# Performance work log

Hardware: AMD Instinct MI355X
Metric: run time of the kernel (lower is better)

## Reference

```python
import jax, jax.numpy as jnp
import numpy as np

N, D_IN = 65536, 512
H1, H2, D_SH = 1024, 1024, 512   # shared net: num_nodes_shared = [1024, 1024, 512]
HI = 512                          # indiv hidden width, num_nodes_indiv = [512, 512]


def setup_inputs() -> dict:
    key = jax.random.key(0)
    ks = jax.random.split(key, 16)
    s = 0.02
    inp = {
        "input": jax.random.normal(ks[0], (N, D_IN), jnp.float32),
        "treatment": jax.random.randint(ks[1], (N,), 0, 2, jnp.int32),
        # shared net (hidden ReLU layers + linear output, all with bias)
        "W0": jax.random.normal(ks[2], (D_IN, H1), jnp.float32) * s,
        "b0": jnp.zeros((H1,), jnp.float32),
        "W1": jax.random.normal(ks[3], (H1, H2), jnp.float32) * s,
        "b1": jnp.zeros((H2,), jnp.float32),
        "W2": jax.random.normal(ks[4], (H2, D_SH), jnp.float32) * s,
        "b2": jnp.zeros((D_SH,), jnp.float32),
        # risk net 0 (output layer has no bias)
        "A0": jax.random.normal(ks[5], (D_SH, HI), jnp.float32) * s,
        "a0": jnp.zeros((HI,), jnp.float32),
        "A1": jax.random.normal(ks[6], (HI, HI), jnp.float32) * s,
        "a1": jnp.zeros((HI,), jnp.float32),
        "A2": jax.random.normal(ks[7], (HI, 1), jnp.float32) * s,
        # risk net 1
        "C0": jax.random.normal(ks[8], (D_SH, HI), jnp.float32) * s,
        "c0": jnp.zeros((HI,), jnp.float32),
        "C1": jax.random.normal(ks[9], (HI, HI), jnp.float32) * s,
        "c1": jnp.zeros((HI,), jnp.float32),
        "C2": jax.random.normal(ks[10], (HI, 1), jnp.float32) * s,
    }
    return inp


def _risk_net(h, U0, u0, U1, u1, U2):
    h = jax.nn.relu(h @ U0 + u0)
    h = jax.nn.relu(h @ U1 + u1)
    return h @ U2  # [N, 1], no output bias


def reference(input, treatment, W0, b0, W1, b1, W2, b2,
              A0, a0, A1, a1, A2, C0, c0, C1, c1, C2):
    # shared MLP
    h = jax.nn.relu(input @ W0 + b0)
    h = jax.nn.relu(h @ W1 + b1)
    out = h @ W2 + b2                     # [N, D_SH]
    # Binary expert routing. The torch code gathers samples per treatment,
    # runs each group through its own MLP and scatters results back; the
    # math is equivalent to applying both experts and selecting per sample.
    y0 = _risk_net(out, A0, a0, A1, a1, A2)[:, 0]  # [N]
    y1 = _risk_net(out, C0, c0, C1, c1, C2)[:, 0]  # [N]
    y = jnp.where(treatment == 0, y0, y1)          # [N]
    return (y, out)
```

## Files before the change

### kernel.cpp

```cpp
#include <hip/hip_runtime.h>
#include <hip/hip_bf16.h>
#include <stdint.h>

typedef short short8 __attribute__((ext_vector_type(8)));
typedef float f32x4 __attribute__((ext_vector_type(4)));

#define NSAMP 65536

__device__ __forceinline__ unsigned short f2bf(float f) {
    union { float f; unsigned u; } v; v.f = f;
    unsigned u = v.u;
    u += 0x7fffu + ((u >> 16) & 1u);
    return (unsigned short)(u >> 16);
}


__global__ void k_convert_bf16(const float* __restrict__ in, unsigned short* __restrict__ out, int n8) {
    int i = blockIdx.x * blockDim.x + threadIdx.x;
    if (i >= n8) return;
    const float4* p = (const float4*)in + (size_t)i * 2;
    float4 a = p[0], b = p[1];
    short8 o;
    o[0] = (short)f2bf(a.x); o[1] = (short)f2bf(a.y);
    o[2] = (short)f2bf(a.z); o[3] = (short)f2bf(a.w);
    o[4] = (short)f2bf(b.x); o[5] = (short)f2bf(b.y);
    o[6] = (short)f2bf(b.z); o[7] = (short)f2bf(b.w);
    ((short8*)out)[i] = o;
}

struct PrepArgs {
    const float *W0, *W1, *W2, *A0, *C0, *A1, *C1, *a0v, *c0v;
    unsigned short *W0T, *W1T, *W2T, *RT0, *A1T, *C1T;
    float *bcat, *y0, *y1;
};
__global__ void k_prep(PrepArgs p) {
    int i = blockIdx.x * blockDim.x + threadIdx.x;
    if (i < 524288)  { int k = i >> 10, n = i & 1023; p.W0T[n * 512 + k] = f2bf(p.W0[i]); return; }
    i -= 524288;
    if (i < 1048576) { int k = i >> 10, n = i & 1023; p.W1T[n * 1024 + k] = f2bf(p.W1[i]); return; }
    i -= 1048576;
    if (i < 524288)  { int k = i >> 9, n = i & 511; p.W2T[n * 1024 + k] = f2bf(p.W2[i]); return; }
    i -= 524288;
    if (i < 262144)  { int k = i >> 9, n = i & 511; p.RT0[n * 512 + k] = f2bf(p.A0[i]); return; }
    i -= 262144;
    if (i < 262144)  { int k = i >> 9, n = i & 511; p.RT0[(512 + n) * 512 + k] = f2bf(p.C0[i]); return; }
    i -= 262144;
    if (i < 262144)  { int k = i >> 9, n = i & 511; p.A1T[n * 512 + k] = f2bf(p.A1[i]); return; }
    i -= 262144;
    if (i < 262144)  { int k = i >> 9, n = i & 511; p.C1T[n * 512 + k] = f2bf(p.C1[i]); return; }
    i -= 262144;
    if (i < 512)     { p.bcat[i] = p.a0v[i]; return; }
    i -= 512;
    if (i < 512)     { p.bcat[512 + i] = p.c0v[i]; return; }
    i -= 512;
    if (i < 65536)   { p.y0[i] = 0.f; return; }
    i -= 65536;
    if (i < 65536)   { p.y1[i] = 0.f; return; }
}

__global__ void k_select(const float* __restrict__ y0, const float* __restrict__ y1,
                         const int* __restrict__ t, float* __restrict__ y, int n) {
    int i = blockIdx.x * blockDim.x + threadIdx.x;
    if (i < n) y[i] = (t[i] == 0) ? y0[i] : y1[i];
}

template<int MODE>
__global__ __launch_bounds__(512, 2)
void k_gemm256(const unsigned short* __restrict__ A, int lda, int colOff,
               const unsigned short* __restrict__ BT,
               const float* __restrict__ bias,
               unsigned short* __restrict__ Cbf,
               float* __restrict__ Cf32,
               const float* __restrict__ w2,
               float* __restrict__ ydot,
               int Ncols, int K, int NB)
{
    __shared__ __align__(16) char lds[131072];

    const int tid  = threadIdx.x;
    const int lane = tid & 63;
    const int wid  = tid >> 6;
    const int wr   = wid >> 2;
    const int wcn  = wid & 3;

    const int nwg = gridDim.x;
    const int bid = blockIdx.x;
    const int swz = (bid & 7) * (nwg >> 3) + (bid >> 3);
    const int mt = swz / NB, nt = swz % NB;
    const int m0 = mt << 8, n0 = nt << 8;

    auto stage = [&](int t, int pb) {
        const int k0 = t << 6;
        char* dA = lds + pb * 65536;
        char* dB = dA + 32768;
#pragma unroll
        for (int q = 0; q < 4; ++q) {
            int chunk = q * 512 + tid;
            int row = chunk >> 3;
            int cs  = (chunk & 7) ^ (row & 7);
            const unsigned short* ga = A + (size_t)(m0 + row) * lda + colOff + k0 + cs * 8;
            char* la = dA + q * 8192 + wid * 1024;
            __builtin_amdgcn_global_load_lds((const __attribute__((address_space(1))) void*)ga,
                                             (__attribute__((address_space(3))) void*)la, 16, 0, 0);
        }
#pragma unroll
        for (int q = 0; q < 4; ++q) {
            int chunk = q * 512 + tid;
            int row = chunk >> 3;
            int cs  = (chunk & 7) ^ (row & 7);
            const unsigned short* gb = BT + (size_t)(n0 + row) * K + k0 + cs * 8;
            char* lb = dB + q * 8192 + wid * 1024;
            __builtin_amdgcn_global_load_lds((const __attribute__((address_space(1))) void*)gb,
                                             (__attribute__((address_space(3))) void*)lb, 16, 0, 0);
        }
    };

    f32x4 acc[8][4];
#pragma unroll
    for (int i = 0; i < 8; ++i)
#pragma unroll
        for (int j = 0; j < 4; ++j) acc[i][j] = (f32x4)0.f;

    const int KT = K >> 6;

    stage(0, 0);
    stage(1, 1);
    asm volatile("s_waitcnt vmcnt(8)" ::: "memory");
    __builtin_amdgcn_s_barrier();
    __builtin_amdgcn_sched_barrier(0);

    for (int t = 0; t < KT; ++t) {
        const char* sA = lds + (t & 1) * 65536;
        const char* sB = sA + 32768;
#pragma unroll
        for (int kk = 0; kk < 2; ++kk) {
            short8 af[8], bfv[4];
#pragma unroll
            for (int i = 0; i < 8; ++i) {
                int r = wr * 128 + i * 16 + (lane & 15);
                int c = (kk * 4 + (lane >> 4)) ^ (r & 7);
                af[i] = *(const short8*)(sA + r * 128 + c * 16);
            }
#pragma unroll
            for (int j = 0; j < 4; ++j) {
                int r = wcn * 64 + j * 16 + (lane & 15);
                int c = (kk * 4 + (lane >> 4)) ^ (r & 7);
                bfv[j] = *(const short8*)(sB + r * 128 + c * 16);
            }
            __builtin_amdgcn_s_setprio(1);
#pragma unroll
            for (int i = 0; i < 8; ++i)
#pragma unroll
                for (int j = 0; j < 4; ++j)
                    acc[i][j] = __builtin_amdgcn_mfma_f32_16x16x32_bf16(af[i], bfv[j], acc[i][j], 0, 0, 0);
            __builtin_amdgcn_s_setprio(0);
        }
        if (t + 1 < KT) {
            __builtin_amdgcn_s_barrier();
            if (t + 2 < KT) {
                stage(t + 2, t & 1);
                asm volatile("s_waitcnt vmcnt(8)" ::: "memory");
            } else {
                asm volatile("s_waitcnt vmcnt(0)" ::: "memory");
            }
            __builtin_amdgcn_s_barrier();
            __builtin_amdgcn_sched_barrier(0);
        }
    }

    const int mbase = m0 + wr * 128 + (lane >> 4) * 4;
    const int nbase = n0 + wcn * 64 + (lane & 15);

    if (MODE == 2) {
        float bv[4], wv[4];
#pragma unroll
        for (int j = 0; j < 4; ++j) {
            int ncol = nbase + j * 16;
            bv[j] = bias[ncol];
            wv[j] = w2[ncol];
        }
#pragma unroll
        for (int i = 0; i < 8; ++i) {
#pragma unroll
            for (int r = 0; r < 4; ++r) {
                float p = 0.f;
#pragma unroll
                for (int j = 0; j < 4; ++j) {
                    float v = fmaxf(acc[i][j][r] + bv[j], 0.f);
                    p += v * wv[j];
                }
                p += __shfl_xor(p, 1);
                p += __shfl_xor(p, 2);
                p += __shfl_xor(p, 4);
                p += __shfl_xor(p, 8);
                if ((lane & 15) == 0) {
                    atomicAdd(&ydot[mbase + i * 16 + r], p);
                }
            }
        }
    } else {
        float bv[4];
#pragma unroll
        for (int j = 0; j < 4; ++j) bv[j] = bias[nbase + j * 16];
#pragma unroll
        for (int i = 0; i < 8; ++i) {
#pragma unroll
            for (int j = 0; j < 4; ++j) {
                int ncol = nbase + j * 16;
#pragma unroll
                for (int r = 0; r < 4; ++r) {
                    float v = acc[i][j][r] + bv[j];
                    if (MODE == 0) v = fmaxf(v, 0.f);
                    size_t idx = (size_t)(mbase + i * 16 + r) * Ncols + ncol;
                    if (MODE == 1) Cf32[idx] = v;
                    Cbf[idx] = f2bf(v);
                }
            }
        }
    }
}


extern "C" void kernel_launch(void* const* d_in, const int* in_sizes, int n_in,
                              void* d_out, int out_size, void* d_ws, size_t ws_size,
                              hipStream_t stream) {
    const float* X  = (const float*)d_in[0];
    const int*  TR  = (const int*)d_in[1];
    const float* W0 = (const float*)d_in[2];  const float* b0 = (const float*)d_in[3];
    const float* W1 = (const float*)d_in[4];  const float* b1 = (const float*)d_in[5];
    const float* W2 = (const float*)d_in[6];  const float* b2 = (const float*)d_in[7];
    const float* A0 = (const float*)d_in[8];  const float* a0 = (const float*)d_in[9];
    const float* A1 = (const float*)d_in[10]; const float* a1 = (const float*)d_in[11];
    const float* A2 = (const float*)d_in[12];
    const float* C0 = (const float*)d_in[13]; const float* c0 = (const float*)d_in[14];
    const float* C1 = (const float*)d_in[15]; const float* c1 = (const float*)d_in[16];
    const float* C2 = (const float*)d_in[17];

    float* y_out   = (float*)d_out;
    float* out_out = (float*)d_out + NSAMP;

    char* ws = (char*)d_ws;
    size_t off = 0;
    auto alloc = [&](size_t bytes) -> char* {
        char* p = ws + off;
        off += (bytes + 255) & ~(size_t)255;
        return p;
    };
    unsigned short* Xb  = (unsigned short*)alloc((size_t)NSAMP * 512 * 2);
    unsigned short* H1b = (unsigned short*)alloc((size_t)NSAMP * 1024 * 2);
    unsigned short* H2b = (unsigned short*)alloc((size_t)NSAMP * 1024 * 2);
    unsigned short* OUTb = H1b;
    unsigned short* R01  = H2b;
    unsigned short* W0T = (unsigned short*)alloc(512 * 1024 * 2);
    unsigned short* W1T = (unsigned short*)alloc(1024 * 1024 * 2);
    unsigned short* W2T = (unsigned short*)alloc(1024 * 512 * 2);
    unsigned short* RT0 = (unsigned short*)alloc(1024 * 512 * 2);
    unsigned short* A1T = (unsigned short*)alloc(512 * 512 * 2);
    unsigned short* C1T = (unsigned short*)alloc(512 * 512 * 2);
    float* bcat = (float*)alloc(1024 * 4);
    float* y0 = (float*)alloc(NSAMP * 4);
    float* y1 = (float*)alloc(NSAMP * 4);

    k_convert_bf16<<<(NSAMP * 512 / 8 + 255) / 256, 256, 0, stream>>>(X, Xb, NSAMP * 512 / 8);
    PrepArgs pa;
    pa.W0 = W0; pa.W1 = W1; pa.W2 = W2; pa.A0 = A0; pa.C0 = C0; pa.A1 = A1; pa.C1 = C1;
    pa.a0v = a0; pa.c0v = c0;
    pa.W0T = W0T; pa.W1T = W1T; pa.W2T = W2T; pa.RT0 = RT0; pa.A1T = A1T; pa.C1T = C1T;
    pa.bcat = bcat; pa.y0 = y0; pa.y1 = y1;
    k_prep<<<(3277824 + 255) / 256, 256, 0, stream>>>(pa);

    const int MB = NSAMP / 256;

    k_gemm256<0><<<MB * 4, 512, 0, stream>>>(Xb, 512, 0, W0T, b0, H1b, nullptr, nullptr, nullptr, 1024, 512, 4);
    k_gemm256<0><<<MB * 4, 512, 0, stream>>>(H1b, 1024, 0, W1T, b1, H2b, nullptr, nullptr, nullptr, 1024, 1024, 4);
    k_gemm256<1><<<MB * 2, 512, 0, stream>>>(H2b, 1024, 0, W2T, b2, OUTb, out_out, nullptr, nullptr, 512, 1024, 2);

    k_gemm256<0><<<MB * 4, 512, 0, stream>>>(OUTb, 512, 0, RT0, bcat, R01, nullptr, nullptr, nullptr, 1024, 512, 4);

    k_gemm256<2><<<MB * 2, 512, 0, stream>>>(R01, 1024, 0,   A1T, a1, nullptr, nullptr, A2, y0, 512, 512, 2);
    k_gemm256<2><<<MB * 2, 512, 0, stream>>>(R01, 1024, 512, C1T, c1, nullptr, nullptr, C2, y1, 512, 512, 2);

    k_select<<<(NSAMP + 255) / 256, 256, 0, stream>>>(y0, y1, TR, y_out, NSAMP);
}
```

Baseline: 578.0 us.

## Restructure GEMM main loop into interleaved half-K phases with finer-grained staging

Splits each 64-wide K tile into two 32-wide halves laid out as separate LDS blocks with a new XOR swizzle, and breaks each iteration into four phases. Each phase issues one slice of the next tile's global-to-LDS loads alongside a subset of fragment reads and MFMAs. The goal is better overlap of memory traffic with matrix math and lower register pressure, since only 4 A fragments are held at a time. In exchange there are many more barriers per iteration and tighter vmcnt accounting, which could add sync overhead or race risk.

```diff
diff --git a/kernel.cpp b/kernel.cpp
--- a/kernel.cpp
+++ b/kernel.cpp
@@ -6,6 +6,8 @@
 typedef float f32x4 __attribute__((ext_vector_type(4)));
 
 #define NSAMP 65536
+#define AS1 __attribute__((address_space(1)))
+#define AS3 __attribute__((address_space(3)))
 
 __device__ __forceinline__ unsigned short f2bf(float f) {
     union { float f; unsigned u; } v; v.f = f;
@@ -89,31 +91,33 @@
     const int mt = swz / NB, nt = swz % NB;
     const int m0 = mt << 8, n0 = nt << 8;
 
-    auto stage = [&](int t, int pb) {
-        const int k0 = t << 6;
-        char* dA = lds + pb * 65536;
-        char* dB = dA + 32768;
-#pragma unroll
-        for (int q = 0; q < 4; ++q) {
-            int chunk = q * 512 + tid;
-            int row = chunk >> 3;
-            int cs  = (chunk & 7) ^ (row & 7);
-            const unsigned short* ga = A + (size_t)(m0 + row) * lda + colOff + k0 + cs * 8;
-            char* la = dA + q * 8192 + wid * 1024;
-            __builtin_amdgcn_global_load_lds((const __attribute__((address_space(1))) void*)ga,
-                                             (__attribute__((address_space(3))) void*)la, 16, 0, 0);
-        }
-#pragma unroll
-        for (int q = 0; q < 4; ++q) {
-            int chunk = q * 512 + tid;
-            int row = chunk >> 3;
-            int cs  = (chunk & 7) ^ (row & 7);
-            const unsigned short* gb = BT + (size_t)(n0 + row) * K + k0 + cs * 8;
-            char* lb = dB + q * 8192 + wid * 1024;
-            __builtin_amdgcn_global_load_lds((const __attribute__((address_space(1))) void*)gb,
-                                             (__attribute__((address_space(3))) void*)lb, 16, 0, 0);
-        }
-    };
+    const int srow = tid >> 2;
+    const int scs  = (tid & 3) ^ ((srow >> 1) & 3);
+    const unsigned short* gA0 = A  + (size_t)(m0 + srow) * lda + colOff + scs * 8;
+    const unsigned short* gA1 = gA0 + (size_t)128 * lda;
+    const unsigned short* gB0 = BT + (size_t)(n0 + srow) * K + scs * 8;
+    const unsigned short* gB1 = gB0 + (size_t)128 * K;
+    const int ldst = wid * 1024;
+
+#define STAGE_BLK(dbuf, blkoff, g0, g1, koff)                                            \
+    do {                                                                                 \
+        __builtin_amdgcn_global_load_lds((const AS1 void*)((g0) + (koff)),               \
+                                         (AS3 void*)((dbuf) + (blkoff) + ldst), 16, 0, 0); \
+        __builtin_amdgcn_global_load_lds((const AS1 void*)((g1) + (koff)),               \
+                                         (AS3 void*)((dbuf) + (blkoff) + 8192 + ldst), 16, 0, 0); \
+    } while (0)
+
+    int aOff[8], bOff[4];
+#pragma unroll
+    for (int i = 0; i < 8; ++i) {
+        int r = wr * 128 + i * 16 + (lane & 15);
+        aOff[i] = r * 64 + ((((lane >> 4) ^ ((r >> 1) & 3))) << 4);
+    }
+#pragma unroll
+    for (int j = 0; j < 4; ++j) {
+        int r = wcn * 64 + j * 16 + (lane & 15);
+        bOff[j] = r * 64 + ((((lane >> 4) ^ ((r >> 1) & 3))) << 4);
+    }
 
     f32x4 acc[8][4];
 #pragma unroll
@@ -123,50 +127,90 @@
 
     const int KT = K >> 6;
 
-    stage(0, 0);
-    stage(1, 1);
-    asm volatile("s_waitcnt vmcnt(8)" ::: "memory");
+    STAGE_BLK(lds, 0,     gA0, gA1, 0);
+    STAGE_BLK(lds, 32768, gB0, gB1, 0);
+    STAGE_BLK(lds, 16384, gA0, gA1, 32);
+    STAGE_BLK(lds, 49152, gB0, gB1, 32);
+    asm volatile("s_waitcnt vmcnt(4)" ::: "memory");
     __builtin_amdgcn_s_barrier();
-    __builtin_amdgcn_sched_barrier(0);
 
     for (int t = 0; t < KT; ++t) {
-        const char* sA = lds + (t & 1) * 65536;
-        const char* sB = sA + 32768;
-#pragma unroll
-        for (int kk = 0; kk < 2; ++kk) {
-            short8 af[8], bfv[4];
-#pragma unroll
-            for (int i = 0; i < 8; ++i) {
-                int r = wr * 128 + i * 16 + (lane & 15);
-                int c = (kk * 4 + (lane >> 4)) ^ (r & 7);
-                af[i] = *(const short8*)(sA + r * 128 + c * 16);
-            }
-#pragma unroll
-            for (int j = 0; j < 4; ++j) {
-                int r = wcn * 64 + j * 16 + (lane & 15);
-                int c = (kk * 4 + (lane >> 4)) ^ (r & 7);
-                bfv[j] = *(const short8*)(sB + r * 128 + c * 16);
-            }
-            __builtin_amdgcn_s_setprio(1);
-#pragma unroll
-            for (int i = 0; i < 8; ++i)
-#pragma unroll
-                for (int j = 0; j < 4; ++j)
-                    acc[i][j] = __builtin_amdgcn_mfma_f32_16x16x32_bf16(af[i], bfv[j], acc[i][j], 0, 0, 0);
-            __builtin_amdgcn_s_setprio(0);
-        }
-        if (t + 1 < KT) {
-            __builtin_amdgcn_s_barrier();
-            if (t + 2 < KT) {
-                stage(t + 2, t & 1);
-                asm volatile("s_waitcnt vmcnt(8)" ::: "memory");
-            } else {
-                asm volatile("s_waitcnt vmcnt(0)" ::: "memory");
-            }
-            __builtin_amdgcn_s_barrier();
-            __builtin_amdgcn_sched_barrier(0);
-        }
+        const char* sbuf = lds + (t & 1) * 65536;
+        char* dbuf = lds + ((t + 1) & 1) * 65536;
+        const int koff = ((t + 1) << 6);
+        const bool st = (t + 1 < KT);
+        short8 af[4], bfv[4];
+
+#pragma unroll
+        for (int i = 0; i < 4; ++i) af[i]  = *(const short8*)(sbuf + aOff[i]);
+#pragma unroll
+        for (int j = 0; j < 4; ++j) bfv[j] = *(const short8*)(sbuf + 32768 + bOff[j]);
+        if (st) STAGE_BLK(dbuf, 0, gA0, gA1, koff);
+        __builtin_amdgcn_s_barrier();
+        asm volatile("s_waitcnt lgkmcnt(0)" ::: "memory");
+        __builtin_amdgcn_sched_barrier(0);
+        __builtin_amdgcn_s_setprio(1);
+#pragma unroll
+        for (int i = 0; i < 4; ++i)
+#pragma unroll
+            for (int j = 0; j < 4; ++j)
+                acc[i][j] = __builtin_amdgcn_mfma_f32_16x16x32_bf16(af[i], bfv[j], acc[i][j], 0, 0, 0);
+        __builtin_amdgcn_s_setprio(0);
+        __builtin_amdgcn_s_barrier();
+
+#pragma unroll
+        for (int i = 0; i < 4; ++i) af[i] = *(const short8*)(sbuf + aOff[4 + i]);
+        if (st) STAGE_BLK(dbuf, 32768, gB0, gB1, koff);
+        __builtin_amdgcn_s_barrier();
+        asm volatile("s_waitcnt lgkmcnt(0)" ::: "memory");
+        __builtin_amdgcn_sched_barrier(0);
+        __builtin_amdgcn_s_setprio(1);
+#pragma unroll
+        for (int i = 0; i < 4; ++i)
+#pragma unroll
+            for (int j = 0; j < 4; ++j)
+                acc[4 + i][j] = __builtin_amdgcn_mfma_f32_16x16x32_bf16(af[i], bfv[j], acc[4 + i][j], 0, 0, 0);
+        __builtin_amdgcn_s_setprio(0);
+        if (st) { asm volatile("s_waitcnt vmcnt(4)" ::: "memory"); }
+        else    { asm volatile("s_waitcnt vmcnt(0)" ::: "memory"); }
+        __builtin_amdgcn_sched_barrier(0);
+        __builtin_amdgcn_s_barrier();
+
+#pragma unroll
+        for (int i = 0; i < 4; ++i) af[i]  = *(const short8*)(sbuf + 16384 + aOff[i]);
+#pragma unroll
+        for (int j = 0; j < 4; ++j) bfv[j] = *(const short8*)(sbuf + 49152 + bOff[j]);
+        if (st) STAGE_BLK(dbuf, 16384, gA0, gA1, koff + 32);
+        __builtin_amdgcn_s_barrier();
+        asm volatile("s_waitcnt lgkmcnt(0)" ::: "memory");
+        __builtin_amdgcn_sched_barrier(0);
+        __builtin_amdgcn_s_setprio(1);
+#pragma unroll
+        for (int i = 0; i < 4; ++i)
+#pragma unroll
+            for (int j = 0; j < 4; ++j)
+                acc[i][j] = __builtin_amdgcn_mfma_f32_16x16x32_bf16(af[i], bfv[j], acc[i][j], 0, 0, 0);
+        __builtin_amdgcn_s_setprio(0);
+        __builtin_amdgcn_s_barrier();
+
+#pragma unroll
+        for (int i = 0; i < 4; ++i) af[i] = *(const short8*)(sbuf + 16384 + aOff[4 + i]);
+        if (st) STAGE_BLK(dbuf, 49152, gB0, gB1, koff + 32);
+        __builtin_amdgcn_s_barrier();
+        asm volatile("s_waitcnt lgkmcnt(0)" ::: "memory");
+        __builtin_amdgcn_sched_barrier(0);
+        __builtin_amdgcn_s_setprio(1);
+#pragma unroll
+        for (int i = 0; i < 4; ++i)
+#pragma unroll
+            for (int j = 0; j < 4; ++j)
+                acc[4 + i][j] = __builtin_amdgcn_mfma_f32_16x16x32_bf16(af[i], bfv[j], acc[4 + i][j], 0, 0, 0);
+        __builtin_amdgcn_s_setprio(0);
+        if (st) { asm volatile("s_waitcnt vmcnt(4)" ::: "memory"); }
+        __builtin_amdgcn_sched_barrier(0);
+        __builtin_amdgcn_s_barrier();
     }
+#undef STAGE_BLK
 
     const int mbase = m0 + wr * 128 + (lane >> 4) * 4;
     const int nbase = n0 + wcn * 64 + (lane & 15);
```

Result: no change. 568.4 us (-1.7%).
